# Kernel tuning notes

Hardware: AMD Instinct MI355X
Metric: run time of the kernel (lower is better)

## Reference

```python
import jax, jax.numpy as jnp
import numpy as np

T, H, I = 8192, 2048, 768  # tokens, hidden_size, intermediate_size

def setup_inputs() -> dict:
    key = jax.random.key(0)
    k1, k2, k3, k4 = jax.random.split(key, 4)
    x = jax.random.normal(k1, (T, H), dtype=jnp.float32)
    # torch nn.Linear weight layout: [out_features, in_features]
    gate_w = jax.random.normal(k2, (I, H), dtype=jnp.float32) * (1.0 / np.sqrt(H))
    up_w = jax.random.normal(k3, (I, H), dtype=jnp.float32) * (1.0 / np.sqrt(H))
    down_w = jax.random.normal(k4, (H, I), dtype=jnp.float32) * (1.0 / np.sqrt(I))
    return {"x": x, "gate_w": gate_w, "up_w": up_w, "down_w": down_w}

def reference(x, gate_w, up_w, down_w):
    # fused SwiGLU MLP: down( silu(x @ gate^T) * (x @ up^T) )
    gate = jnp.einsum('th,ih->ti', x, gate_w)   # [T, I]
    up = jnp.einsum('th,ih->ti', x, up_w)       # [T, I]
    h = jax.nn.silu(gate) * up                   # [T, I]
    out = jnp.einsum('ti,hi->th', h, down_w)     # [T, H]
    return out
```

## Files before the change

### kernel.cpp

```cpp
#include <hip/hip_runtime.h>
#include <hip/hip_bf16.h>
#include <stdint.h>

#define T_DIM 8192
#define H_DIM 2048
#define I_DIM 768

typedef __bf16 bf16_t;
typedef bf16_t bf16x8 __attribute__((ext_vector_type(8)));
typedef bf16_t bf16x4 __attribute__((ext_vector_type(4)));
typedef float  f32x4  __attribute__((ext_vector_type(4)));

__device__ __forceinline__ void async_load16(const void* g, void* s) {
    __builtin_amdgcn_global_load_lds(
        (const __attribute__((address_space(1))) void*)g,
        (__attribute__((address_space(3))) void*)s, 16, 0, 0);
}

__device__ __forceinline__ void phase_barrier() {
    asm volatile("" ::: "memory");
    __builtin_amdgcn_s_barrier();
    asm volatile("" ::: "memory");
}

__device__ __forceinline__ bf16x8 cvt8(float4 a, float4 b) {
    bf16x8 o;
    o[0] = (bf16_t)a.x; o[1] = (bf16_t)a.y; o[2] = (bf16_t)a.z; o[3] = (bf16_t)a.w;
    o[4] = (bf16_t)b.x; o[5] = (bf16_t)b.y; o[6] = (bf16_t)b.z; o[7] = (bf16_t)b.w;
    return o;
}

__global__ __launch_bounds__(256) void cvt_kernel(
    const float* __restrict__ X, const float* __restrict__ G,
    const float* __restrict__ U, const float* __restrict__ D,
    bf16_t* __restrict__ Xb, bf16_t* __restrict__ Gb,
    bf16_t* __restrict__ Ub, bf16_t* __restrict__ Db)
{
    const size_t N8X = (size_t)T_DIM * H_DIM / 8;
    const size_t N8W = (size_t)I_DIM * H_DIM / 8;
    const size_t total = N8X + 3 * N8W;
    for (size_t i = (size_t)blockIdx.x * blockDim.x + threadIdx.x; i < total;
         i += (size_t)gridDim.x * blockDim.x) {
        const float* s; bf16_t* d; size_t j = i;
        if (j < N8X) { s = X; d = Xb; }
        else {
            j -= N8X;
            if (j < N8W) { s = G; d = Gb; }
            else { j -= N8W;
                if (j < N8W) { s = U; d = Ub; }
                else { j -= N8W; s = D; d = Db; } }
        }
        float4 v0 = ((const float4*)s)[2 * j];
        float4 v1 = ((const float4*)s)[2 * j + 1];
        ((bf16x8*)d)[j] = cvt8(v0, v1);
    }
}

__global__ __launch_bounds__(256) void gateup_kernel(
    const bf16_t* __restrict__ X,
    const bf16_t* __restrict__ Wg,
    const bf16_t* __restrict__ Wu,
    bf16_t* __restrict__ Hbuf)
{
    __shared__ __align__(16) bf16_t sA[128 * 32];
    __shared__ __align__(16) bf16_t sG[64 * 32];
    __shared__ __align__(16) bf16_t sU[64 * 32];

    const int tid   = threadIdx.x;
    const int lane  = tid & 63;
    const int wave  = tid >> 6;
    const int waveM = wave >> 1;
    const int waveN = wave & 1;
    const int quad  = lane >> 4;
    const int lrow  = lane & 15;

    const int blockM = blockIdx.x;
    const int blockN = blockIdx.y;

    f32x4 accG[4][2], accU[4][2];
#pragma unroll
    for (int i = 0; i < 4; i++)
#pragma unroll
        for (int j = 0; j < 2; j++) { accG[i][j] = (f32x4)(0.f); accU[i][j] = (f32x4)(0.f); }

    const int s0 = tid, s1 = tid + 256;
    const int rA0 = s0 >> 2, cA0 = (s0 & 3) * 8;
    const int rA1 = s1 >> 2, cA1 = (s1 & 3) * 8;
    const int rW  = tid >> 2, cW  = (tid & 3) * 8;

    const bf16_t* Ab = X  + (size_t)(blockM * 128) * H_DIM;
    const bf16_t* Gb = Wg + (size_t)(blockN * 64) * H_DIM;
    const bf16_t* Ub = Wu + (size_t)(blockN * 64) * H_DIM;

    for (int k0 = 0; k0 < H_DIM; k0 += 32) {
        async_load16(Ab + (size_t)rA0 * H_DIM + k0 + cA0, &sA[s0 * 8]);
        async_load16(Ab + (size_t)rA1 * H_DIM + k0 + cA1, &sA[s1 * 8]);
        async_load16(Gb + (size_t)rW  * H_DIM + k0 + cW,  &sG[tid * 8]);
        async_load16(Ub + (size_t)rW  * H_DIM + k0 + cW,  &sU[tid * 8]);
        __syncthreads();

        bf16x8 aF[4], gF[2], uF[2];
#pragma unroll
        for (int mi = 0; mi < 4; mi++) {
            int r = waveM * 64 + mi * 16 + lrow;
            aF[mi] = *(const bf16x8*)&sA[r * 32 + quad * 8];
        }
#pragma unroll
        for (int ni = 0; ni < 2; ni++) {
            int r = waveN * 32 + ni * 16 + lrow;
            gF[ni] = *(const bf16x8*)&sG[r * 32 + quad * 8];
            uF[ni] = *(const bf16x8*)&sU[r * 32 + quad * 8];
        }
        __syncthreads();

#pragma unroll
        for (int mi = 0; mi < 4; mi++)
#pragma unroll
            for (int ni = 0; ni < 2; ni++) {
                accG[mi][ni] = __builtin_amdgcn_mfma_f32_16x16x32_bf16(aF[mi], gF[ni], accG[mi][ni], 0, 0, 0);
                accU[mi][ni] = __builtin_amdgcn_mfma_f32_16x16x32_bf16(aF[mi], uF[ni], accU[mi][ni], 0, 0, 0);
            }
    }

#pragma unroll
    for (int mi = 0; mi < 4; mi++) {
#pragma unroll
        for (int ni = 0; ni < 2; ni++) {
#pragma unroll
            for (int r = 0; r < 4; r++) {
                int row = blockM * 128 + waveM * 64 + mi * 16 + quad * 4 + r;
                int col = blockN * 64 + waveN * 32 + ni * 16 + lrow;
                float g = accG[mi][ni][r];
                float u = accU[mi][ni][r];
                float h = (g / (1.f + __expf(-g))) * u;
                Hbuf[(size_t)row * I_DIM + col] = (bf16_t)h;
            }
        }
    }
}

__global__ __launch_bounds__(512, 2) void down_kernel(
    const bf16_t* __restrict__ Hbuf,
    const bf16_t* __restrict__ Wd,
    float* __restrict__ Out)
{
    __shared__ __align__(16) bf16_t sA[2][256 * 64];
    __shared__ __align__(16) bf16_t sB[2][256 * 64];

    const int tid  = threadIdx.x;
    const int lane = tid & 63;
    const int wave = tid >> 6;
    const int wm   = wave >> 2;
    const int wn   = wave & 3;
    const int quad = lane >> 4;
    const int lrow = lane & 15;

    const int bm = blockIdx.x;
    const int bn = blockIdx.y;

    f32x4 acc[8][4];
#pragma unroll
    for (int i = 0; i < 8; i++)
#pragma unroll
        for (int j = 0; j < 4; j++) acc[i][j] = (f32x4)(0.f);

    int stRow[4], stCol[4];
#pragma unroll
    for (int i = 0; i < 4; i++) {
        int s = tid + 512 * i;
        stRow[i] = s >> 3;
        stCol[i] = ((s & 7) ^ ((s >> 3) & 7)) * 8;
    }

    const bf16_t* Ab = Hbuf + (size_t)(bm * 256) * I_DIM;
    const bf16_t* Bb = Wd   + (size_t)(bn * 256) * I_DIM;

#define STAGE_A(t) do { _Pragma("unroll") \
    for (int i_ = 0; i_ < 4; i_++) \
        async_load16(Ab + (size_t)stRow[i_] * I_DIM + (t) * 64 + stCol[i_], \
                     &sA[(t) & 1][(tid + 512 * i_) * 8]); } while (0)
#define STAGE_B(t) do { _Pragma("unroll") \
    for (int i_ = 0; i_ < 4; i_++) \
        async_load16(Bb + (size_t)stRow[i_] * I_DIM + (t) * 64 + stCol[i_], \
                     &sB[(t) & 1][(tid + 512 * i_) * 8]); } while (0)

    int aOff[8], bOff[4];
#pragma unroll
    for (int mi = 0; mi < 8; mi++) {
        int r = wm * 128 + mi * 16 + lrow;
        aOff[mi] = r * 64 + ((quad ^ (r & 7)) * 8);
    }
#pragma unroll
    for (int ni = 0; ni < 4; ni++) {
        int r = wn * 64 + ni * 16 + lrow;
        bOff[ni] = r * 64 + ((quad ^ (r & 7)) * 8);
    }

    const int nt = I_DIM / 64;

    STAGE_A(0); STAGE_B(0); STAGE_B(1);
    asm volatile("s_waitcnt vmcnt(4)" ::: "memory");
    phase_barrier();

    for (int t = 0; t < nt; ++t) {
        const int p = t & 1;
        bf16x8 bF[4][2];

#pragma unroll
        for (int q = 0; q < 4; ++q) {
            bf16x8 aF[2][2];
            if (q == 0) {
#pragma unroll
                for (int ni = 0; ni < 4; ni++) {
                    bF[ni][0] = *(const bf16x8*)&sB[p][bOff[ni]];
                    bF[ni][1] = *(const bf16x8*)&sB[p][bOff[ni] ^ 32];
                }
            }
#pragma unroll
            for (int j = 0; j < 2; j++) {
                aF[j][0] = *(const bf16x8*)&sA[p][aOff[2 * q + j]];
                aF[j][1] = *(const bf16x8*)&sA[p][aOff[2 * q + j] ^ 32];
            }
            if (q == 0 && t + 1 < nt) STAGE_A(t + 1);
            if (q == 1 && t + 2 < nt) STAGE_B(t + 2);

            phase_barrier();
            asm volatile("s_waitcnt lgkmcnt(0)" ::: "memory");
            __builtin_amdgcn_sched_barrier(0);
            __builtin_amdgcn_s_setprio(1);
#pragma unroll
            for (int j = 0; j < 2; j++)
#pragma unroll
                for (int ni = 0; ni < 4; ni++)
#pragma unroll
                    for (int kk = 0; kk < 2; kk++)
                        acc[2 * q + j][ni] = __builtin_amdgcn_mfma_f32_16x16x32_bf16(
                            aF[j][kk], bF[ni][kk], acc[2 * q + j][ni], 0, 0, 0);
            __builtin_amdgcn_s_setprio(0);
            if (q < 3) phase_barrier();
        }

        if (t < nt - 2) {
            asm volatile("s_waitcnt vmcnt(4)" ::: "memory");
            phase_barrier();
        } else if (t == nt - 2) {
            asm volatile("s_waitcnt vmcnt(0)" ::: "memory");
            phase_barrier();
        }
    }
#undef STAGE_A
#undef STAGE_B

#pragma unroll
    for (int mi = 0; mi < 8; mi++) {
#pragma unroll
        for (int ni = 0; ni < 4; ni++) {
#pragma unroll
            for (int r = 0; r < 4; r++) {
                int row = bm * 256 + wm * 128 + mi * 16 + quad * 4 + r;
                int col = bn * 256 + wn * 64 + ni * 16 + lrow;
                Out[(size_t)row * H_DIM + col] = acc[mi][ni][r];
            }
        }
    }
}

extern "C" void kernel_launch(void* const* d_in, const int* in_sizes, int n_in,
                              void* d_out, int out_size, void* d_ws, size_t ws_size,
                              hipStream_t stream) {
    const float* x  = (const float*)d_in[0];
    const float* gw = (const float*)d_in[1];
    const float* uw = (const float*)d_in[2];
    const float* dw = (const float*)d_in[3];
    float* out = (float*)d_out;

    bf16_t* xb = (bf16_t*)d_ws;
    bf16_t* gb = xb + (size_t)T_DIM * H_DIM;
    bf16_t* ub = gb + (size_t)I_DIM * H_DIM;
    bf16_t* db = ub + (size_t)I_DIM * H_DIM;
    bf16_t* hb = db + (size_t)I_DIM * H_DIM;

    cvt_kernel<<<2048, 256, 0, stream>>>(x, gw, uw, dw, xb, gb, ub, db);
    gateup_kernel<<<dim3(T_DIM / 128, I_DIM / 64), 256, 0, stream>>>(xb, gb, ub, hb);
    down_kernel<<<dim3(T_DIM / 256, H_DIM / 256), 512, 0, stream>>>(hb, db, out);
}
```

Measured before the change: 221.5 us.

## Rewrite gate/up GEMM with 256x256 tiles, double-buffered async loads and swizzled LDS

Replaces the simple 128x64 gate/up kernel, which used a single buffer and two syncs per 32-wide K step, with a 512-thread 256x256 tile kernel. Gate and up weight rows are interleaved in 16-row groups so one B tile covers both. The new kernel stages 64-wide K slices into double-buffered LDS with an XOR swizzle and overlaps prefetch with MFMA using waitcnt, barrier and setprio scheduling. The aim is better data reuse, fewer bank conflicts and hidden global load latency, at the cost of higher register and LDS pressure and fragile manual vmcnt accounting.

```diff
diff --git a/kernel.cpp b/kernel.cpp
--- a/kernel.cpp
+++ b/kernel.cpp
@@ -56,82 +56,130 @@
     }
 }
 
-__global__ __launch_bounds__(256) void gateup_kernel(
+__global__ __launch_bounds__(512, 2) void gateup_kernel(
     const bf16_t* __restrict__ X,
     const bf16_t* __restrict__ Wg,
     const bf16_t* __restrict__ Wu,
     bf16_t* __restrict__ Hbuf)
 {
-    __shared__ __align__(16) bf16_t sA[128 * 32];
-    __shared__ __align__(16) bf16_t sG[64 * 32];
-    __shared__ __align__(16) bf16_t sU[64 * 32];
-
-    const int tid   = threadIdx.x;
-    const int lane  = tid & 63;
-    const int wave  = tid >> 6;
-    const int waveM = wave >> 1;
-    const int waveN = wave & 1;
-    const int quad  = lane >> 4;
-    const int lrow  = lane & 15;
-
-    const int blockM = blockIdx.x;
-    const int blockN = blockIdx.y;
-
-    f32x4 accG[4][2], accU[4][2];
-#pragma unroll
-    for (int i = 0; i < 4; i++)
-#pragma unroll
-        for (int j = 0; j < 2; j++) { accG[i][j] = (f32x4)(0.f); accU[i][j] = (f32x4)(0.f); }
-
-    const int s0 = tid, s1 = tid + 256;
-    const int rA0 = s0 >> 2, cA0 = (s0 & 3) * 8;
-    const int rA1 = s1 >> 2, cA1 = (s1 & 3) * 8;
-    const int rW  = tid >> 2, cW  = (tid & 3) * 8;
-
-    const bf16_t* Ab = X  + (size_t)(blockM * 128) * H_DIM;
-    const bf16_t* Gb = Wg + (size_t)(blockN * 64) * H_DIM;
-    const bf16_t* Ub = Wu + (size_t)(blockN * 64) * H_DIM;
-
-    for (int k0 = 0; k0 < H_DIM; k0 += 32) {
-        async_load16(Ab + (size_t)rA0 * H_DIM + k0 + cA0, &sA[s0 * 8]);
-        async_load16(Ab + (size_t)rA1 * H_DIM + k0 + cA1, &sA[s1 * 8]);
-        async_load16(Gb + (size_t)rW  * H_DIM + k0 + cW,  &sG[tid * 8]);
-        async_load16(Ub + (size_t)rW  * H_DIM + k0 + cW,  &sU[tid * 8]);
-        __syncthreads();
-
-        bf16x8 aF[4], gF[2], uF[2];
-#pragma unroll
-        for (int mi = 0; mi < 4; mi++) {
-            int r = waveM * 64 + mi * 16 + lrow;
-            aF[mi] = *(const bf16x8*)&sA[r * 32 + quad * 8];
-        }
-#pragma unroll
-        for (int ni = 0; ni < 2; ni++) {
-            int r = waveN * 32 + ni * 16 + lrow;
-            gF[ni] = *(const bf16x8*)&sG[r * 32 + quad * 8];
-            uF[ni] = *(const bf16x8*)&sU[r * 32 + quad * 8];
-        }
-        __syncthreads();
-
-#pragma unroll
-        for (int mi = 0; mi < 4; mi++)
-#pragma unroll
-            for (int ni = 0; ni < 2; ni++) {
-                accG[mi][ni] = __builtin_amdgcn_mfma_f32_16x16x32_bf16(aF[mi], gF[ni], accG[mi][ni], 0, 0, 0);
-                accU[mi][ni] = __builtin_amdgcn_mfma_f32_16x16x32_bf16(aF[mi], uF[ni], accU[mi][ni], 0, 0, 0);
-            }
-    }
-
-#pragma unroll
-    for (int mi = 0; mi < 4; mi++) {
-#pragma unroll
-        for (int ni = 0; ni < 2; ni++) {
+    __shared__ __align__(16) bf16_t sA[2][256 * 64];
+    __shared__ __align__(16) bf16_t sB[2][256 * 64];
+
+    const int tid  = threadIdx.x;
+    const int lane = tid & 63;
+    const int wave = tid >> 6;
+    const int wm   = wave >> 2;
+    const int wn   = wave & 3;
+    const int quad = lane >> 4;
+    const int lrow = lane & 15;
+
+    const int bm = blockIdx.x;
+    const int bn = blockIdx.y;
+
+    f32x4 acc[8][4];
+#pragma unroll
+    for (int i = 0; i < 8; i++)
+#pragma unroll
+        for (int j = 0; j < 4; j++) acc[i][j] = (f32x4)(0.f);
+
+    const bf16_t* aSrc[4];
+    const bf16_t* bSrc[4];
+#pragma unroll
+    for (int i = 0; i < 4; i++) {
+        int s = tid + 512 * i;
+        int r = s >> 3;
+        int c = ((s & 7) ^ (r & 7)) * 8;
+        aSrc[i] = X + (size_t)(bm * 256 + r) * H_DIM + c;
+        int g = r >> 5, w = r & 31;
+        const bf16_t* wb = (w < 16) ? Wg : Wu;
+        aSrc[i] = aSrc[i];
+        bSrc[i] = wb + (size_t)(bn * 128 + g * 16 + (w & 15)) * H_DIM + c;
+    }
+
+#define STAGE_A(t) do { _Pragma("unroll") \
+    for (int i_ = 0; i_ < 4; i_++) \
+        async_load16(aSrc[i_] + (t) * 64, &sA[(t) & 1][(tid + 512 * i_) * 8]); } while (0)
+#define STAGE_B(t) do { _Pragma("unroll") \
+    for (int i_ = 0; i_ < 4; i_++) \
+        async_load16(bSrc[i_] + (t) * 64, &sB[(t) & 1][(tid + 512 * i_) * 8]); } while (0)
+
+    int aOff[8], bOff[4];
+#pragma unroll
+    for (int mi = 0; mi < 8; mi++) {
+        int r = wm * 128 + mi * 16 + lrow;
+        aOff[mi] = r * 64 + ((quad ^ (r & 7)) * 8);
+    }
+#pragma unroll
+    for (int ni = 0; ni < 4; ni++) {
+        int r = wn * 64 + ni * 16 + lrow;
+        bOff[ni] = r * 64 + ((quad ^ (r & 7)) * 8);
+    }
+
+    const int nt = H_DIM / 64;
+
+    STAGE_A(0); STAGE_B(0); STAGE_B(1);
+    asm volatile("s_waitcnt vmcnt(4)" ::: "memory");
+    phase_barrier();
+
+    for (int t = 0; t < nt; ++t) {
+        const int p = t & 1;
+        bf16x8 bF[4][2];
+
+#pragma unroll
+        for (int q = 0; q < 4; ++q) {
+            bf16x8 aF[2][2];
+            if (q == 0) {
+#pragma unroll
+                for (int ni = 0; ni < 4; ni++) {
+                    bF[ni][0] = *(const bf16x8*)&sB[p][bOff[ni]];
+                    bF[ni][1] = *(const bf16x8*)&sB[p][bOff[ni] ^ 32];
+                }
+            }
+#pragma unroll
+            for (int j = 0; j < 2; j++) {
+                aF[j][0] = *(const bf16x8*)&sA[p][aOff[2 * q + j]];
+                aF[j][1] = *(const bf16x8*)&sA[p][aOff[2 * q + j] ^ 32];
+            }
+            if (q == 0 && t + 1 < nt) STAGE_A(t + 1);
+            if (q == 1 && t + 2 < nt) STAGE_B(t + 2);
+
+            phase_barrier();
+            asm volatile("s_waitcnt lgkmcnt(0)" ::: "memory");
+            __builtin_amdgcn_sched_barrier(0);
+            __builtin_amdgcn_s_setprio(1);
+#pragma unroll
+            for (int j = 0; j < 2; j++)
+#pragma unroll
+                for (int ni = 0; ni < 4; ni++)
+#pragma unroll
+                    for (int kk = 0; kk < 2; kk++)
+                        acc[2 * q + j][ni] = __builtin_amdgcn_mfma_f32_16x16x32_bf16(
+                            aF[j][kk], bF[ni][kk], acc[2 * q + j][ni], 0, 0, 0);
+            __builtin_amdgcn_s_setprio(0);
+            if (q < 3) phase_barrier();
+        }
+
+        if (t < nt - 2) {
+            asm volatile("s_waitcnt vmcnt(4)" ::: "memory");
+            phase_barrier();
+        } else if (t == nt - 2) {
+            asm volatile("s_waitcnt vmcnt(0)" ::: "memory");
+            phase_barrier();
+        }
+    }
+#undef STAGE_A
+#undef STAGE_B
+
+#pragma unroll
+    for (int mi = 0; mi < 8; mi++) {
+#pragma unroll
+        for (int k = 0; k < 2; k++) {
 #pragma unroll
             for (int r = 0; r < 4; r++) {
-                int row = blockM * 128 + waveM * 64 + mi * 16 + quad * 4 + r;
-                int col = blockN * 64 + waveN * 32 + ni * 16 + lrow;
-                float g = accG[mi][ni][r];
-                float u = accU[mi][ni][r];
+                int row = bm * 256 + wm * 128 + mi * 16 + quad * 4 + r;
+                int col = bn * 128 + wn * 32 + k * 16 + lrow;
+                float g = acc[mi][2 * k][r];
+                float u = acc[mi][2 * k + 1][r];
                 float h = (g / (1.f + __expf(-g))) * u;
                 Hbuf[(size_t)row * I_DIM + col] = (bf16_t)h;
             }
@@ -281,6 +329,6 @@
     bf16_t* hb = db + (size_t)I_DIM * H_DIM;
 
     cvt_kernel<<<2048, 256, 0, stream>>>(x, gw, uw, dw, xb, gb, ub, db);
-    gateup_kernel<<<dim3(T_DIM / 128, I_DIM / 64), 256, 0, stream>>>(xb, gb, ub, hb);
+    gateup_kernel<<<dim3(T_DIM / 256, I_DIM / 128), 512, 0, stream>>>(xb, gb, ub, hb);
     down_kernel<<<dim3(T_DIM / 256, H_DIM / 256), 512, 0, stream>>>(hb, db, out);
 }
```

Measured after the change: 227.0 us. 2.4% more time.
